# Kernel tuning notes

Measured on AMD Instinct MI355X. Metric: run time of the kernel, lower is better.

Reference implementation:

```python
import jax, jax.numpy as jnp
import numpy as np

B, N, HID = 1, 2048, 1024
H, WK, WV = 16, 64, 64
DH = HID // H  # 64


def setup_inputs() -> dict:
    key = jax.random.key(0)
    ks = jax.random.split(key, 10)
    s = 0.02
    return {
        "hidden_states": jax.random.normal(ks[0], (B, N, HID), jnp.float32),
        "attention_mask": jnp.ones((B, N), jnp.float32),
        "Wq": jax.random.normal(ks[1], (HID, HID), jnp.float32) * s,
        "bq": jnp.zeros((HID,), jnp.float32),
        "Wk": jax.random.normal(ks[2], (HID, HID), jnp.float32) * s,
        "bk": jnp.zeros((HID,), jnp.float32),
        "Wv": jax.random.normal(ks[3], (HID, HID), jnp.float32) * s,
        "bv": jnp.zeros((HID,), jnp.float32),
        # Conv1D(2*WK+1, DH, bias=False): weight [nx=DH, nf=2*WK+1]
        "W_rel_k": jax.random.normal(ks[4], (DH, 2 * WK + 1), jnp.float32) * s,
        # relative_pos_val: [2*WV+1, DH]
        "W_rel_v": jax.random.normal(ks[5], (2 * WV + 1, DH), jnp.float32) * s,
    }


def _attention(hidden_states, attention_mask, Wq, bq, Wk, bk, Wv, bv, W_rel_k, W_rel_v):
    b, n, _ = hidden_states.shape

    def heads(x):  # [B,N,HID] -> [B,H,N,DH]
        return x.reshape(b, n, H, DH).transpose(0, 2, 1, 3)

    q = heads(hidden_states @ Wq + bq)
    k = heads(hidden_states @ Wk + bk)
    v = heads(hidden_states @ Wv + bv)

    scores = jnp.einsum("bhid,bhjd->bhij", q, k)  # [B,H,N,N]

    # --- relative-position key bias: bias[i, j] = q_i . w_{j-i+WK} for |j-i|<=WK ---
    a_k = jnp.einsum("bhid,dw->bhiw", q, W_rel_k)  # [B,H,N,2*WK+1]
    rows = jnp.arange(n)
    slot = rows[None, :] - rows[:, None] + WK       # [N,N] relative slot j-i+WK
    valid_k = (slot >= 0) & (slot <= 2 * WK)
    bias = a_k[:, :, rows[:, None], jnp.clip(slot, 0, 2 * WK)]  # [B,H,N,N]
    scores = scores + jnp.where(valid_k, bias, 0.0)

    scores = scores / np.float32(np.sqrt(DH))  # temperature == 1.0

    # extended attention mask: (1 - mask) * dtype_min added to scores
    ext = (1.0 - attention_mask)[:, None, None, :] * jnp.finfo(scores.dtype).min
    scores = scores + ext

    probs = jax.nn.softmax(scores, axis=-1)  # [B,H,N,N]

    ctx = jnp.einsum("bhij,bhjd->bhid", probs, v)  # [B,H,N,DH]

    # --- relative-position value: band[i, r] = probs[i, i-WV+r]; ctx += band @ W_rel_v ---
    offs = jnp.arange(2 * WV + 1)
    kpos = rows[:, None] - WV + offs[None, :]       # [N, 2*WV+1] absolute key position
    valid_v = (kpos >= 0) & (kpos < n)
    band = probs[:, :, rows[:, None], jnp.clip(kpos, 0, n - 1)]  # [B,H,N,2*WV+1]
    band = jnp.where(valid_v, band, 0.0)
    ctx = ctx + jnp.einsum("bhiw,wd->bhid", band, W_rel_v)

    # merge heads -> [B,N,HID]
    return ctx.transpose(0, 2, 1, 3).reshape(b, n, HID)


def reference(hidden_states, attention_mask, Wq, bq, Wk, bk, Wv, bv, W_rel_k, W_rel_v):
    return _attention(hidden_states, attention_mask, Wq, bq, Wk, bk, Wv, bv, W_rel_k, W_rel_v)
```

## Files before the change

kernel.cpp:

```cpp
#include <hip/hip_runtime.h>
#include <hip/hip_bf16.h>

#define NSEQ 2048
#define HIDDIM 1024
#define NH 16
#define DHEAD 64
#define NW 129
#define AKS 132

typedef float          f32x4 __attribute__((ext_vector_type(4)));
typedef _Float16       f16x4 __attribute__((ext_vector_type(4)));
typedef _Float16       f16x8 __attribute__((ext_vector_type(8)));
typedef unsigned short u16x8 __attribute__((ext_vector_type(8)));
typedef unsigned short u16;

__device__ __forceinline__ float b2f(u16 u){ return __uint_as_float(((unsigned)u) << 16); }
__device__ __forceinline__ float ld_any(const void* p, long idx, int flag){
  return flag ? b2f(((const u16*)p)[idx]) : ((const float*)p)[idx];
}

#define GLOAD_LDS16(gp, lp) \
  __builtin_amdgcn_global_load_lds((const __attribute__((address_space(1))) unsigned int*)(gp), \
                                   (__attribute__((address_space(3))) unsigned int*)(lp), 16, 0, 0)

static const size_t OFF_Q    = 0;
static const size_t OFF_K    = (size_t)4  << 20;
static const size_t OFF_VT   = (size_t)8  << 20;
static const size_t OFF_WT   = (size_t)12 << 20;
static const size_t OFF_AK   = (size_t)18 << 20;
static const size_t OFF_M    = OFF_AK + (size_t)NH * NSEQ * AKS * 4;
static const size_t OFF_L    = OFF_M + (size_t)2 * NH * NSEQ * 4;
static const size_t OFF_CTXP = OFF_L + (size_t)2 * NH * NSEQ * 4;
static const size_t OFF_HSF  = OFF_CTXP + (size_t)2 * NSEQ * HIDDIM * 4;
static const size_t OFF_BIAS = OFF_HSF + (size_t)NSEQ * HIDDIM * 2;
static const size_t OFF_WRK  = OFF_BIAS + 3 * 1024 * 4;
static const size_t OFF_WRV  = OFF_WRK + (size_t)DHEAD * NW * 4;
static const size_t OFF_EXT  = OFF_WRV + (size_t)NW * DHEAD * 4;
static const size_t OFF_FLAG = OFF_EXT + (size_t)NSEQ * 4;

__global__ void detect_kernel(const unsigned* __restrict__ mask_raw, int* __restrict__ flagp){
  *flagp = (mask_raw[0] == 0x3F800000u) ? 0 : 1;
}

__global__ void cvt_hs_kernel(const void* __restrict__ hs, const int* __restrict__ flagp,
                              _Float16* __restrict__ hsf){
  const int flag = *flagp;
  const long base = (long)(blockIdx.x * 256 + threadIdx.x) * 8;
  f16x8 o;
  if (flag){
    const u16* b = (const u16*)hs;
#pragma unroll
    for (int e = 0; e < 8; e++) o[e] = (_Float16)b2f(b[base + e]);
  } else {
    const float* f = (const float*)hs;
#pragma unroll
    for (int e = 0; e < 8; e++) o[e] = (_Float16)f[base + e];
  }
  *(f16x8*)(hsf + base) = o;
}

__global__ void cvt_small_kernel(const void* __restrict__ bq, const void* __restrict__ bk,
                                 const void* __restrict__ bv, const void* __restrict__ wrk,
                                 const void* __restrict__ wrv, const void* __restrict__ mask,
                                 const int* __restrict__ flagp,
                                 float* __restrict__ biasf, float* __restrict__ wrkf,
                                 float* __restrict__ wrvf, float* __restrict__ extf){
  const int flag = *flagp;
  const int idx = blockIdx.x * 256 + threadIdx.x;
  if (idx < 1024)            biasf[idx] = ld_any(bq, idx, flag);
  else if (idx < 2048)       biasf[idx] = ld_any(bk, idx - 1024, flag);
  else if (idx < 3072)       biasf[idx] = ld_any(bv, idx - 2048, flag);
  else if (idx < 3072 + 8256)  wrkf[idx - 3072]  = ld_any(wrk, idx - 3072, flag);
  else if (idx < 3072 + 16512) wrvf[idx - 11328] = ld_any(wrv, idx - 11328, flag);
  else if (idx < 3072 + 16512 + 2048)
    extf[idx - 19584] = (1.f - ld_any(mask, idx - 19584, flag)) * -1.0e30f;
}

__global__ void wtrans_kernel(const void* __restrict__ Wq, const void* __restrict__ Wk,
                              const void* __restrict__ Wv, const int* __restrict__ flagp,
                              _Float16* __restrict__ Wt){
  __shared__ __attribute__((aligned(16))) _Float16 tile[64][65];
  const int flag = *flagp;
  const int z = blockIdx.z;
  const void* src = (z == 0) ? Wq : ((z == 1) ? Wk : Wv);
  _Float16* dst = Wt + (size_t)z * 1024 * 1024;
  const int o0 = blockIdx.x * 64, k0 = blockIdx.y * 64;
  const int t = threadIdx.x;
#pragma unroll
  for (int c = 0; c < 2; c++){
    int idx = t + 256 * c;
    int r = idx >> 3, c8 = (idx & 7) * 8;
    long off = (long)(k0 + r) * 1024 + o0 + c8;
#pragma unroll
    for (int e = 0; e < 8; e++) tile[r][c8 + e] = (_Float16)ld_any(src, off + e, flag);
  }
  __syncthreads();
#pragma unroll
  for (int c = 0; c < 2; c++){
    int idx = t + 256 * c;
    int orow = idx >> 3, k8 = (idx & 7) * 8;
    f16x8 v;
#pragma unroll
    for (int e = 0; e < 8; e++) v[e] = tile[k8 + e][orow];
    *(f16x8*)(dst + (size_t)(o0 + orow) * 1024 + k0 + k8) = v;
  }
}

__launch_bounds__(256, 2)
__global__ void qkv_kernel(const _Float16* __restrict__ hsf, const _Float16* __restrict__ Wt,
                           const float* __restrict__ biasf,
                           _Float16* __restrict__ Qf, _Float16* __restrict__ Kf,
                           _Float16* __restrict__ Vtf){
  __shared__ __attribute__((aligned(16))) _Float16 As[128 * 40];
  __shared__ __attribute__((aligned(16))) _Float16 Bs[128 * 40];
  const int z = blockIdx.z;
  const _Float16* Wz = Wt + (size_t)z * 1024 * 1024;
  const int o0 = blockIdx.x * 128, m0 = blockIdx.y * 128;
  const int t = threadIdx.x, lane = t & 63, wave = t >> 6;
  const int wm = wave >> 1, wn = wave & 1;
  const int q = lane >> 4, ln = lane & 15;
  f32x4 acc[4][4];
#pragma unroll
  for (int a = 0; a < 4; a++)
#pragma unroll
    for (int b = 0; b < 4; b++) acc[a][b] = (f32x4){0.f, 0.f, 0.f, 0.f};

  for (int k0 = 0; k0 < 1024; k0 += 32){
#pragma unroll
    for (int c = 0; c < 2; c++){
      int idx = t + 256 * c;
      int r = idx >> 2, col = (idx & 3) * 8;
      *(f16x8*)&As[r * 40 + col] = *(const f16x8*)(hsf + (size_t)(m0 + r) * 1024 + k0 + col);
      *(f16x8*)&Bs[r * 40 + col] = *(const f16x8*)(Wz + (size_t)(o0 + r) * 1024 + k0 + col);
    }
    __syncthreads();
    f16x8 af[4], bf[4];
#pragma unroll
    for (int mt = 0; mt < 4; mt++) af[mt] = *(const f16x8*)&As[(wm * 64 + mt * 16 + ln) * 40 + q * 8];
#pragma unroll
    for (int nt = 0; nt < 4; nt++) bf[nt] = *(const f16x8*)&Bs[(wn * 64 + nt * 16 + ln) * 40 + q * 8];
#pragma unroll
    for (int mt = 0; mt < 4; mt++)
#pragma unroll
      for (int nt = 0; nt < 4; nt++)
        acc[mt][nt] = __builtin_amdgcn_mfma_f32_16x16x32_f16(af[mt], bf[nt], acc[mt][nt], 0, 0, 0);
    __syncthreads();
  }
#pragma unroll
  for (int nt = 0; nt < 4; nt++){
    int o = o0 + wn * 64 + nt * 16 + ln;
    float bval = biasf[z * 1024 + o];
    int hh = o >> 6, dd = o & 63;
#pragma unroll
    for (int mt = 0; mt < 4; mt++){
      int nb = m0 + wm * 64 + mt * 16 + q * 4;
      if (z == 2){
        f16x4 pk;
#pragma unroll
        for (int r = 0; r < 4; r++) pk[r] = (_Float16)(acc[mt][nt][r] + bval);
        *(f16x4*)(Vtf + (size_t)(hh * 64 + dd) * 2048 + nb) = pk;
      } else {
        _Float16* dstp = (z == 0) ? Qf : Kf;
#pragma unroll
        for (int r = 0; r < 4; r++)
          dstp[(size_t)(hh * 2048 + nb + r) * 64 + dd] = (_Float16)(acc[mt][nt][r] + bval);
      }
    }
  }
}

__launch_bounds__(256, 2)
__global__ void ak_kernel(const _Float16* __restrict__ Qf, const float* __restrict__ wrkf,
                          float* __restrict__ ak){
  __shared__ __attribute__((aligned(16))) _Float16 WrkT[144 * 72];
  const int h = blockIdx.y;
  const int i0 = blockIdx.x * 128;
  const int t = threadIdx.x, lane = t & 63, wave = t >> 6;
  const int q = lane >> 4, ln = lane & 15;
  for (int c = 0; c < 36; c++){
    int idx = t + 256 * c;
    int w = idx >> 6, d = idx & 63;
    float v = (w < NW) ? wrkf[d * NW + w] : 0.f;
    WrkT[w * 72 + d] = (_Float16)v;
  }
  __syncthreads();
  f16x8 afr[2][2];
#pragma unroll
  for (int mt = 0; mt < 2; mt++){
    int row = i0 + wave * 32 + mt * 16 + ln;
#pragma unroll
    for (int ks = 0; ks < 2; ks++)
      afr[mt][ks] = *(const f16x8*)(Qf + (size_t)(h * 2048 + row) * 64 + ks * 32 + q * 8);
  }
  f32x4 acc[2][9];
#pragma unroll
  for (int a = 0; a < 2; a++)
#pragma unroll
    for (int b = 0; b < 9; b++) acc[a][b] = (f32x4){0.f, 0.f, 0.f, 0.f};
#pragma unroll
  for (int nt = 0; nt < 9; nt++){
    f16x8 bfr0 = *(const f16x8*)&WrkT[(nt * 16 + ln) * 72 + q * 8];
    f16x8 bfr1 = *(const f16x8*)&WrkT[(nt * 16 + ln) * 72 + 32 + q * 8];
#pragma unroll
    for (int mt = 0; mt < 2; mt++){
      acc[mt][nt] = __builtin_amdgcn_mfma_f32_16x16x32_f16(afr[mt][0], bfr0, acc[mt][nt], 0, 0, 0);
      acc[mt][nt] = __builtin_amdgcn_mfma_f32_16x16x32_f16(afr[mt][1], bfr1, acc[mt][nt], 0, 0, 0);
    }
  }
#pragma unroll
  for (int nt = 0; nt < 9; nt++){
    int w = nt * 16 + ln;
    if (w > 128) continue;
#pragma unroll
    for (int mt = 0; mt < 2; mt++){
      int ib = i0 + wave * 32 + mt * 16 + q * 4;
#pragma unroll
      for (int r = 0; r < 4; r++)
        ak[(size_t)(h * 2048 + ib + r) * AKS + w] = acc[mt][nt][r];
    }
  }
}

__launch_bounds__(256, 4)
__global__ void flash_kernel(const float* __restrict__ extf,
                             const _Float16* __restrict__ Qf, const _Float16* __restrict__ Kf,
                             const _Float16* __restrict__ Vtf, float* akm,
                             float* __restrict__ ctxpart, float* __restrict__ mws,
                             float* __restrict__ lws){
  __shared__ __attribute__((aligned(16))) _Float16 Ks[2 * 64 * 64];
  __shared__ __attribute__((aligned(16))) _Float16 Vts[2 * 64 * 64];
  __shared__ __attribute__((aligned(16))) float Exts[1024];
  const int h = blockIdx.x, qt = blockIdx.y, jh = blockIdx.z;
  const int t = threadIdx.x, lane = t & 63, wave = t >> 6;
  const int q = lane >> 4, ln = lane & 15;
  const int ibase = qt * 64 + wave * 16;
  const int i = ibase + ln;

  auto stage = [&](int nb, int jn){
#pragma unroll
    for (int s2 = 0; s2 < 2; s2++){
      const int g = s2 * 256 + t;
      const int row = g >> 3, slot = g & 7;
      const int col8 = slot ^ (row & 7);
      const _Float16* gK = Kf + (((size_t)(h * 2048 + jn + row)) << 6) + (col8 << 3);
      const _Float16* gV = Vtf + (((size_t)(h * 64 + row)) << 11) + jn + (col8 << 3);
      _Float16* lK = (_Float16*)Ks + nb * 4096 + ((s2 * 4 + wave) << 9);
      _Float16* lV = (_Float16*)Vts + nb * 4096 + ((s2 * 4 + wave) << 9);
      GLOAD_LDS16(gK, lK);
      GLOAD_LDS16(gV, lV);
    }
  };

  f16x8 qfrag[2];
  {
    const _Float16* qrow = Qf + (size_t)(h * 2048 + i) * 64;
    qfrag[0] = *(const f16x8*)(qrow + q * 8);
    qfrag[1] = *(const f16x8*)(qrow + 32 + q * 8);
  }
  f32x4 accc[4];
#pragma unroll
  for (int dt = 0; dt < 4; dt++) accc[dt] = (f32x4){0.f, 0.f, 0.f, 0.f};
  float m_i = -1.0e30f, l_i = 0.f;
  float* akrow = akm + (size_t)(h * 2048 + i) * AKS;

#pragma unroll
  for (int c2 = 0; c2 < 4; c2++) Exts[t + 256 * c2] = extf[jh * 1024 + t + 256 * c2];
  stage(0, jh * 1024);
  __syncthreads();

  int cur = 0;
  for (int jt = 0; jt < 16; ++jt){
    const int j0 = jh * 1024 + jt * 64;
    if (jt < 15) stage(cur ^ 1, j0 + 64);

    const _Float16* KsC = (const _Float16*)Ks + cur * 4096;
    const _Float16* VsC = (const _Float16*)Vts + cur * 4096;

    f32x4 s[4];
    __builtin_amdgcn_s_setprio(1);
#pragma unroll
    for (int mt = 0; mt < 4; mt++){
      const int row = mt * 16 + ln, rs = row & 7;
      f16x8 kf0 = *(const f16x8*)&KsC[(row << 6) + ((q ^ rs) << 3)];
      f16x8 kf1 = *(const f16x8*)&KsC[(row << 6) + (((q + 4) ^ rs) << 3)];
      f32x4 zz = (f32x4){0.f, 0.f, 0.f, 0.f};
      zz = __builtin_amdgcn_mfma_f32_16x16x32_f16(kf0, qfrag[0], zz, 0, 0, 0);
      zz = __builtin_amdgcn_mfma_f32_16x16x32_f16(kf1, qfrag[1], zz, 0, 0, 0);
      s[mt] = zz;
    }
    __builtin_amdgcn_s_setprio(0);

    const bool band = (j0 <= ibase + 79) && (j0 + 63 >= ibase - 64);
#pragma unroll
    for (int mt = 0; mt < 4; mt++){
      f32x4 ev = *(const f32x4*)&Exts[jt * 64 + mt * 16 + (q << 2)];
#pragma unroll
      for (int r = 0; r < 4; r++){
        float x = s[mt][r];
        int w = j0 + mt * 16 + (q << 2) + r - i + 64;
        if (band && (unsigned)w <= 128u){
          x = (x + akrow[w]) * 0.125f + ev[r];
          akrow[w] = x;
        } else {
          x = x * 0.125f + ev[r];
        }
        s[mt][r] = x;
      }
    }

    float tmax = -1.0e30f;
#pragma unroll
    for (int mt = 0; mt < 4; mt++)
#pragma unroll
      for (int r = 0; r < 4; r++) tmax = fmaxf(tmax, s[mt][r]);
    tmax = fmaxf(tmax, __shfl_xor(tmax, 16, 64));
    tmax = fmaxf(tmax, __shfl_xor(tmax, 32, 64));
    float mnew = fmaxf(m_i, tmax);
    if (!__all(tmax <= m_i)){
      float alpha = __expf(m_i - mnew);
      l_i *= alpha;
#pragma unroll
      for (int dt = 0; dt < 4; dt++)
#pragma unroll
        for (int r = 0; r < 4; r++) accc[dt][r] *= alpha;
    }
    m_i = mnew;
    float tsum = 0.f;
    f16x4 pf[4];
#pragma unroll
    for (int mt = 0; mt < 4; mt++)
#pragma unroll
      for (int r = 0; r < 4; r++){
        float p = __expf(s[mt][r] - mnew);
        tsum += p;
        pf[mt][r] = (_Float16)p;
      }
    tsum += __shfl_xor(tsum, 16, 64);
    tsum += __shfl_xor(tsum, 32, 64);
    l_i += tsum;

    __builtin_amdgcn_s_setprio(1);
#pragma unroll
    for (int dt = 0; dt < 4; dt++){
      const int d = dt * 16 + ln, ds7 = d & 7;
#pragma unroll
      for (int ks = 0; ks < 4; ks++){
        const int c8 = ((ks << 1) | (q >> 1)) ^ ds7;
        f16x4 vf = *(const f16x4*)&VsC[(d << 6) + (c8 << 3) + ((q & 1) << 2)];
        accc[dt] = __builtin_amdgcn_mfma_f32_16x16x16f16(vf, pf[ks], accc[dt], 0, 0, 0);
      }
    }
    __builtin_amdgcn_s_setprio(0);

    __syncthreads();
    cur ^= 1;
  }

  float* cdst = ctxpart + (size_t)jh * NSEQ * HIDDIM;
#pragma unroll
  for (int dt = 0; dt < 4; dt++)
    *(f32x4*)(cdst + (size_t)i * 1024 + h * 64 + dt * 16 + q * 4) = accc[dt];
  if (q == 0){
    mws[jh * NH * NSEQ + h * 2048 + i] = m_i;
    lws[jh * NH * NSEQ + h * 2048 + i] = l_i;
  }
}

__launch_bounds__(256, 2)
__global__ void finish_kernel(const float* __restrict__ sband, const float* __restrict__ mws,
                              const float* __restrict__ lws, const float* __restrict__ wrvf,
                              const float* __restrict__ ctxpart, float* __restrict__ out){
  __shared__ __attribute__((aligned(16))) _Float16 WrvT[64 * 144];
  __shared__ __attribute__((aligned(16))) _Float16 pT[144 * 72];
  __shared__ __attribute__((aligned(16))) float sM[64], sIL[64], sC0[64], sC1[64];
  const int qt = blockIdx.x, h = blockIdx.y;
  const int i0 = qt * 64;
  const int t = threadIdx.x, lane = t & 63, wave = t >> 6;
  const int q = lane >> 4, ln = lane & 15;
  for (int c = 0; c < 36; c++){
    int idx = c * 256 + t;
    int w = idx >> 6, d = idx & 63;
    WrvT[d * 144 + w] = (w < NW) ? (_Float16)wrvf[w * 64 + d] : (_Float16)0.f;
  }
  if (t < 64){
    int i = i0 + t;
    float m0 = mws[h * 2048 + i],            m1 = mws[NH * NSEQ + h * 2048 + i];
    float l0 = lws[h * 2048 + i],            l1 = lws[NH * NSEQ + h * 2048 + i];
    float M = fmaxf(m0, m1);
    float a0 = __expf(m0 - M), a1 = __expf(m1 - M);
    float L = a0 * l0 + a1 * l1;
    float iL = 1.f / L;
    sM[t] = M; sIL[t] = iL; sC0[t] = a0 * iL; sC1[t] = a1 * iL;
  }
  __syncthreads();
  for (int ii = 0; ii < 16; ii++){
    int il = wave * 16 + ii;
    float Mv = sM[il], ILv = sIL[il];
    const float* srow = sband + (size_t)(h * 2048 + i0 + il) * AKS;
#pragma unroll
    for (int c = 0; c < 3; c++){
      int w = lane + 64 * c;
      if (w < 144){
        float p = (w < NW) ? __expf(srow[w] - Mv) * ILv : 0.f;
        pT[w * 72 + il] = (_Float16)p;
      }
    }
  }
  __syncthreads();
  f32x4 acc[4];
#pragma unroll
  for (int mt = 0; mt < 4; mt++) acc[mt] = (f32x4){0.f, 0.f, 0.f, 0.f};
#pragma unroll
  for (int ks = 0; ks < 9; ks++){
    f16x4 bfr;
#pragma unroll
    for (int j = 0; j < 4; j++) bfr[j] = pT[(ks * 16 + q * 4 + j) * 72 + wave * 16 + ln];
#pragma unroll
    for (int mt = 0; mt < 4; mt++){
      f16x4 afr = *(const f16x4*)&WrvT[(mt * 16 + ln) * 144 + ks * 16 + q * 4];
      acc[mt] = __builtin_amdgcn_mfma_f32_16x16x16f16(afr, bfr, acc[mt], 0, 0, 0);
    }
  }
  const int i = i0 + wave * 16 + ln;
  const float c0 = sC0[wave * 16 + ln], c1 = sC1[wave * 16 + ln];
  const float* p0 = ctxpart;
  const float* p1 = ctxpart + (size_t)NSEQ * HIDDIM;
#pragma unroll
  for (int mt = 0; mt < 4; mt++){
    size_t off = (size_t)i * 1024 + h * 64 + mt * 16 + q * 4;
    f32x4 A0 = *(const f32x4*)(p0 + off);
    f32x4 A1 = *(const f32x4*)(p1 + off);
    f32x4 o4;
#pragma unroll
    for (int r = 0; r < 4; r++) o4[r] = c0 * A0[r] + c1 * A1[r] + acc[mt][r];
    *(f32x4*)(out + off) = o4;
  }
}

extern "C" void kernel_launch(void* const* d_in, const int* in_sizes, int n_in,
                              void* d_out, int out_size, void* d_ws, size_t ws_size,
                              hipStream_t stream){
  const void* hs   = d_in[0];
  const void* mask = d_in[1];
  const void* Wq   = d_in[2];
  const void* bq   = d_in[3];
  const void* Wk   = d_in[4];
  const void* bk   = d_in[5];
  const void* Wv   = d_in[6];
  const void* bv   = d_in[7];
  const void* Wrk  = d_in[8];
  const void* Wrv  = d_in[9];
  float* out = (float*)d_out;

  char* ws = (char*)d_ws;
  _Float16* Qf    = (_Float16*)(ws + OFF_Q);
  _Float16* Kf    = (_Float16*)(ws + OFF_K);
  _Float16* Vtf   = (_Float16*)(ws + OFF_VT);
  _Float16* Wt    = (_Float16*)(ws + OFF_WT);
  float*    akp   = (float*)   (ws + OFF_AK);
  float*    mp    = (float*)   (ws + OFF_M);
  float*    lp    = (float*)   (ws + OFF_L);
  float*    ctxp  = (float*)   (ws + OFF_CTXP);
  _Float16* hsf   = (_Float16*)(ws + OFF_HSF);
  float*    biasf = (float*)   (ws + OFF_BIAS);
  float*    wrkf  = (float*)   (ws + OFF_WRK);
  float*    wrvf  = (float*)   (ws + OFF_WRV);
  float*    extf  = (float*)   (ws + OFF_EXT);
  int*      flagp = (int*)     (ws + OFF_FLAG);

  detect_kernel   <<<dim3(1),          1,   0, stream>>>((const unsigned*)mask, flagp);
  cvt_hs_kernel   <<<dim3(1024),       256, 0, stream>>>(hs, flagp, hsf);
  cvt_small_kernel<<<dim3(85),         256, 0, stream>>>(bq, bk, bv, Wrk, Wrv, mask, flagp,
                                                         biasf, wrkf, wrvf, extf);
  wtrans_kernel   <<<dim3(16, 16, 3),  256, 0, stream>>>(Wq, Wk, Wv, flagp, Wt);
  qkv_kernel      <<<dim3(8, 16, 3),   256, 0, stream>>>(hsf, Wt, biasf, Qf, Kf, Vtf);
  ak_kernel       <<<dim3(16, 16),     256, 0, stream>>>(Qf, wrkf, akp);
  flash_kernel    <<<dim3(16, 32, 2),  256, 0, stream>>>(extf, Qf, Kf, Vtf, akp, ctxp, mp, lp);
  finish_kernel   <<<dim3(32, 16),     256, 0, stream>>>(akp, mp, lp, wrvf, ctxp, out);
}
```

Before: 208.0 us.

## Pipeline QKV GEMM with async LDS loads and split flash keys four ways

The QKV GEMM moves to direct global-to-LDS double-buffered loads with 64-row tiles and MFMA priority hints. The 1/sqrt(d) scale is folded into Q at projection time, which removes per-score multiplies in the flash kernel. The flash kernel now uses 512-thread blocks over 128 query rows and splits keys into four chunks, with the finish kernel merging four partials. A fast path skips band logic for off-band tiles, and the workspace is re-laid out so the weight and half-precision input buffers alias the context partial region.

```diff
diff --git a/kernel.cpp b/kernel.cpp
--- a/kernel.cpp
+++ b/kernel.cpp
@@ -7,11 +7,11 @@
 #define DHEAD 64
 #define NW 129
 #define AKS 132
+#define NSPLIT 4
 
 typedef float          f32x4 __attribute__((ext_vector_type(4)));
 typedef _Float16       f16x4 __attribute__((ext_vector_type(4)));
 typedef _Float16       f16x8 __attribute__((ext_vector_type(8)));
-typedef unsigned short u16x8 __attribute__((ext_vector_type(8)));
 typedef unsigned short u16;
 
 __device__ __forceinline__ float b2f(u16 u){ return __uint_as_float(((unsigned)u) << 16); }
@@ -26,13 +26,13 @@
 static const size_t OFF_Q    = 0;
 static const size_t OFF_K    = (size_t)4  << 20;
 static const size_t OFF_VT   = (size_t)8  << 20;
-static const size_t OFF_WT   = (size_t)12 << 20;
-static const size_t OFF_AK   = (size_t)18 << 20;
+static const size_t OFF_AK   = (size_t)12 << 20;
 static const size_t OFF_M    = OFF_AK + (size_t)NH * NSEQ * AKS * 4;
-static const size_t OFF_L    = OFF_M + (size_t)2 * NH * NSEQ * 4;
-static const size_t OFF_CTXP = OFF_L + (size_t)2 * NH * NSEQ * 4;
-static const size_t OFF_HSF  = OFF_CTXP + (size_t)2 * NSEQ * HIDDIM * 4;
-static const size_t OFF_BIAS = OFF_HSF + (size_t)NSEQ * HIDDIM * 2;
+static const size_t OFF_L    = OFF_M + (size_t)NSPLIT * NH * NSEQ * 4;
+static const size_t OFF_CTXP = OFF_L + (size_t)NSPLIT * NH * NSEQ * 4;
+static const size_t OFF_WT   = OFF_CTXP;
+static const size_t OFF_HSF  = OFF_CTXP + ((size_t)6 << 20);
+static const size_t OFF_BIAS = OFF_CTXP + (size_t)NSPLIT * NSEQ * HIDDIM * 4;
 static const size_t OFF_WRK  = OFF_BIAS + 3 * 1024 * 4;
 static const size_t OFF_WRV  = OFF_WRK + (size_t)DHEAD * NW * 4;
 static const size_t OFF_EXT  = OFF_WRV + (size_t)NW * DHEAD * 4;
@@ -106,54 +106,74 @@
   }
 }
 
-__launch_bounds__(256, 2)
+__launch_bounds__(256, 3)
 __global__ void qkv_kernel(const _Float16* __restrict__ hsf, const _Float16* __restrict__ Wt,
                            const float* __restrict__ biasf,
                            _Float16* __restrict__ Qf, _Float16* __restrict__ Kf,
                            _Float16* __restrict__ Vtf){
-  __shared__ __attribute__((aligned(16))) _Float16 As[128 * 40];
-  __shared__ __attribute__((aligned(16))) _Float16 Bs[128 * 40];
+  __shared__ __attribute__((aligned(16))) _Float16 As[2 * 64 * 32];
+  __shared__ __attribute__((aligned(16))) _Float16 Bs[2 * 128 * 32];
   const int z = blockIdx.z;
   const _Float16* Wz = Wt + (size_t)z * 1024 * 1024;
-  const int o0 = blockIdx.x * 128, m0 = blockIdx.y * 128;
+  const int o0 = blockIdx.x * 128, m0 = blockIdx.y * 64;
   const int t = threadIdx.x, lane = t & 63, wave = t >> 6;
   const int wm = wave >> 1, wn = wave & 1;
   const int q = lane >> 4, ln = lane & 15;
-  f32x4 acc[4][4];
-#pragma unroll
-  for (int a = 0; a < 4; a++)
+
+  auto stage = [&](int nb, int k0){
+    {
+      const int row = t >> 2, chunk = t & 3;
+      const _Float16* gA = hsf + (size_t)(m0 + row) * 1024 + k0 + chunk * 8;
+      _Float16* lA = (_Float16*)As + nb * 2048 + (wave << 9);
+      GLOAD_LDS16(gA, lA);
+    }
+#pragma unroll
+    for (int p = 0; p < 2; p++){
+      const int idx = p * 256 + t;
+      const int row = idx >> 2, chunk = idx & 3;
+      const _Float16* gB = Wz + (size_t)(o0 + row) * 1024 + k0 + chunk * 8;
+      _Float16* lB = (_Float16*)Bs + nb * 4096 + ((p * 4 + wave) << 9);
+      GLOAD_LDS16(gB, lB);
+    }
+  };
+
+  f32x4 acc[2][4];
+#pragma unroll
+  for (int a = 0; a < 2; a++)
 #pragma unroll
     for (int b = 0; b < 4; b++) acc[a][b] = (f32x4){0.f, 0.f, 0.f, 0.f};
 
+  stage(0, 0);
+  __syncthreads();
+  int cur = 0;
   for (int k0 = 0; k0 < 1024; k0 += 32){
-#pragma unroll
-    for (int c = 0; c < 2; c++){
-      int idx = t + 256 * c;
-      int r = idx >> 2, col = (idx & 3) * 8;
-      *(f16x8*)&As[r * 40 + col] = *(const f16x8*)(hsf + (size_t)(m0 + r) * 1024 + k0 + col);
-      *(f16x8*)&Bs[r * 40 + col] = *(const f16x8*)(Wz + (size_t)(o0 + r) * 1024 + k0 + col);
-    }
-    __syncthreads();
-    f16x8 af[4], bf[4];
-#pragma unroll
-    for (int mt = 0; mt < 4; mt++) af[mt] = *(const f16x8*)&As[(wm * 64 + mt * 16 + ln) * 40 + q * 8];
-#pragma unroll
-    for (int nt = 0; nt < 4; nt++) bf[nt] = *(const f16x8*)&Bs[(wn * 64 + nt * 16 + ln) * 40 + q * 8];
-#pragma unroll
-    for (int mt = 0; mt < 4; mt++)
+    if (k0 + 32 < 1024) stage(cur ^ 1, k0 + 32);
+    const _Float16* Ac = (const _Float16*)As + cur * 2048;
+    const _Float16* Bc = (const _Float16*)Bs + cur * 4096;
+    f16x8 af[2], bf[4];
+#pragma unroll
+    for (int mt = 0; mt < 2; mt++) af[mt] = *(const f16x8*)&Ac[(wm * 32 + mt * 16 + ln) * 32 + q * 8];
+#pragma unroll
+    for (int nt = 0; nt < 4; nt++) bf[nt] = *(const f16x8*)&Bc[(wn * 64 + nt * 16 + ln) * 32 + q * 8];
+    __builtin_amdgcn_s_setprio(1);
+#pragma unroll
+    for (int mt = 0; mt < 2; mt++)
 #pragma unroll
       for (int nt = 0; nt < 4; nt++)
         acc[mt][nt] = __builtin_amdgcn_mfma_f32_16x16x32_f16(af[mt], bf[nt], acc[mt][nt], 0, 0, 0);
+    __builtin_amdgcn_s_setprio(0);
     __syncthreads();
-  }
+    cur ^= 1;
+  }
+  const float sc = (z == 0) ? 0.125f : 1.0f;
 #pragma unroll
   for (int nt = 0; nt < 4; nt++){
     int o = o0 + wn * 64 + nt * 16 + ln;
     float bval = biasf[z * 1024 + o];
     int hh = o >> 6, dd = o & 63;
 #pragma unroll
-    for (int mt = 0; mt < 4; mt++){
-      int nb = m0 + wm * 64 + mt * 16 + q * 4;
+    for (int mt = 0; mt < 2; mt++){
+      int nb = m0 + wm * 32 + mt * 16 + q * 4;
       if (z == 2){
         f16x4 pk;
 #pragma unroll
@@ -163,7 +183,7 @@
         _Float16* dstp = (z == 0) ? Qf : Kf;
 #pragma unroll
         for (int r = 0; r < 4; r++)
-          dstp[(size_t)(hh * 2048 + nb + r) * 64 + dd] = (_Float16)(acc[mt][nt][r] + bval);
+          dstp[(size_t)(hh * 2048 + nb + r) * 64 + dd] = (_Float16)((acc[mt][nt][r] + bval) * sc);
       }
     }
   }
@@ -221,7 +241,7 @@
   }
 }
 
-__launch_bounds__(256, 4)
+__launch_bounds__(512, 8)
 __global__ void flash_kernel(const float* __restrict__ extf,
                              const _Float16* __restrict__ Qf, const _Float16* __restrict__ Kf,
                              const _Float16* __restrict__ Vtf, float* akm,
@@ -229,26 +249,22 @@
                              float* __restrict__ lws){
   __shared__ __attribute__((aligned(16))) _Float16 Ks[2 * 64 * 64];
   __shared__ __attribute__((aligned(16))) _Float16 Vts[2 * 64 * 64];
-  __shared__ __attribute__((aligned(16))) float Exts[1024];
+  __shared__ __attribute__((aligned(16))) float Exts[512];
   const int h = blockIdx.x, qt = blockIdx.y, jh = blockIdx.z;
   const int t = threadIdx.x, lane = t & 63, wave = t >> 6;
   const int q = lane >> 4, ln = lane & 15;
-  const int ibase = qt * 64 + wave * 16;
+  const int ibase = qt * 128 + wave * 16;
   const int i = ibase + ln;
 
   auto stage = [&](int nb, int jn){
-#pragma unroll
-    for (int s2 = 0; s2 < 2; s2++){
-      const int g = s2 * 256 + t;
-      const int row = g >> 3, slot = g & 7;
-      const int col8 = slot ^ (row & 7);
-      const _Float16* gK = Kf + (((size_t)(h * 2048 + jn + row)) << 6) + (col8 << 3);
-      const _Float16* gV = Vtf + (((size_t)(h * 64 + row)) << 11) + jn + (col8 << 3);
-      _Float16* lK = (_Float16*)Ks + nb * 4096 + ((s2 * 4 + wave) << 9);
-      _Float16* lV = (_Float16*)Vts + nb * 4096 + ((s2 * 4 + wave) << 9);
-      GLOAD_LDS16(gK, lK);
-      GLOAD_LDS16(gV, lV);
-    }
+    const int row = t >> 3, slot = t & 7;
+    const int col8 = slot ^ (row & 7);
+    const _Float16* gK = Kf + (((size_t)(h * 2048 + jn + row)) << 6) + (col8 << 3);
+    const _Float16* gV = Vtf + (((size_t)(h * 64 + row)) << 11) + jn + (col8 << 3);
+    _Float16* lK = (_Float16*)Ks + nb * 4096 + (wave << 9);
+    _Float16* lV = (_Float16*)Vts + nb * 4096 + (wave << 9);
+    GLOAD_LDS16(gK, lK);
+    GLOAD_LDS16(gV, lV);
   };
 
   f16x8 qfrag[2];
@@ -263,15 +279,14 @@
   float m_i = -1.0e30f, l_i = 0.f;
   float* akrow = akm + (size_t)(h * 2048 + i) * AKS;
 
-#pragma unroll
-  for (int c2 = 0; c2 < 4; c2++) Exts[t + 256 * c2] = extf[jh * 1024 + t + 256 * c2];
-  stage(0, jh * 1024);
+  Exts[t] = extf[jh * 512 + t];
+  stage(0, jh * 512);
   __syncthreads();
 
   int cur = 0;
-  for (int jt = 0; jt < 16; ++jt){
-    const int j0 = jh * 1024 + jt * 64;
-    if (jt < 15) stage(cur ^ 1, j0 + 64);
+  for (int jt = 0; jt < 8; ++jt){
+    const int j0 = jh * 512 + jt * 64;
+    if (jt < 7) stage(cur ^ 1, j0 + 64);
 
     const _Float16* KsC = (const _Float16*)Ks + cur * 4096;
     const _Float16* VsC = (const _Float16*)Vts + cur * 4096;
@@ -291,20 +306,29 @@
     __builtin_amdgcn_s_setprio(0);
 
     const bool band = (j0 <= ibase + 79) && (j0 + 63 >= ibase - 64);
-#pragma unroll
-    for (int mt = 0; mt < 4; mt++){
-      f32x4 ev = *(const f32x4*)&Exts[jt * 64 + mt * 16 + (q << 2)];
-#pragma unroll
-      for (int r = 0; r < 4; r++){
-        float x = s[mt][r];
-        int w = j0 + mt * 16 + (q << 2) + r - i + 64;
-        if (band && (unsigned)w <= 128u){
-          x = (x + akrow[w]) * 0.125f + ev[r];
-          akrow[w] = x;
-        } else {
-          x = x * 0.125f + ev[r];
+    if (band){
+#pragma unroll
+      for (int mt = 0; mt < 4; mt++){
+        f32x4 ev = *(const f32x4*)&Exts[jt * 64 + mt * 16 + (q << 2)];
+#pragma unroll
+        for (int r = 0; r < 4; r++){
+          float x = s[mt][r];
+          int w = j0 + mt * 16 + (q << 2) + r - i + 64;
+          if ((unsigned)w <= 128u){
+            x = x + akrow[w] + ev[r];
+            akrow[w] = x;
+          } else {
+            x = x + ev[r];
+          }
+          s[mt][r] = x;
         }
-        s[mt][r] = x;
+      }
+    } else {
+#pragma unroll
+      for (int mt = 0; mt < 4; mt++){
+        f32x4 ev = *(const f32x4*)&Exts[jt * 64 + mt * 16 + (q << 2)];
+#pragma unroll
+        for (int r = 0; r < 4; r++) s[mt][r] += ev[r];
       }
     }
 
@@ -372,7 +396,7 @@
                               const float* __restrict__ ctxpart, float* __restrict__ out){
   __shared__ __attribute__((aligned(16))) _Float16 WrvT[64 * 144];
   __shared__ __attribute__((aligned(16))) _Float16 pT[144 * 72];
-  __shared__ __attribute__((aligned(16))) float sM[64], sIL[64], sC0[64], sC1[64];
+  __shared__ __attribute__((aligned(16))) float sM[64], sIL[64], sC[NSPLIT][64];
   const int qt = blockIdx.x, h = blockIdx.y;
   const int i0 = qt * 64;
   const int t = threadIdx.x, lane = t & 63, wave = t >> 6;
@@ -384,13 +408,20 @@
   }
   if (t < 64){
     int i = i0 + t;
-    float m0 = mws[h * 2048 + i],            m1 = mws[NH * NSEQ + h * 2048 + i];
-    float l0 = lws[h * 2048 + i],            l1 = lws[NH * NSEQ + h * 2048 + i];
-    float M = fmaxf(m0, m1);
-    float a0 = __expf(m0 - M), a1 = __expf(m1 - M);
-    float L = a0 * l0 + a1 * l1;
+    float mv[NSPLIT], lv[NSPLIT];
+#pragma unroll
+    for (int jj = 0; jj < NSPLIT; jj++){
+      mv[jj] = mws[jj * NH * NSEQ + h * 2048 + i];
+      lv[jj] = lws[jj * NH * NSEQ + h * 2048 + i];
+    }
+    float M = fmaxf(fmaxf(mv[0], mv[1]), fmaxf(mv[2], mv[3]));
+    float L = 0.f, a[NSPLIT];
+#pragma unroll
+    for (int jj = 0; jj < NSPLIT; jj++){ a[jj] = __expf(mv[jj] - M); L += a[jj] * lv[jj]; }
     float iL = 1.f / L;
-    sM[t] = M; sIL[t] = iL; sC0[t] = a0 * iL; sC1[t] = a1 * iL;
+    sM[t] = M; sIL[t] = iL;
+#pragma unroll
+    for (int jj = 0; jj < NSPLIT; jj++) sC[jj][t] = a[jj] * iL;
   }
   __syncthreads();
   for (int ii = 0; ii < 16; ii++){
@@ -422,17 +453,18 @@
     }
   }
   const int i = i0 + wave * 16 + ln;
-  const float c0 = sC0[wave * 16 + ln], c1 = sC1[wave * 16 + ln];
-  const float* p0 = ctxpart;
-  const float* p1 = ctxpart + (size_t)NSEQ * HIDDIM;
+  const int il = wave * 16 + ln;
+  const float c0 = sC[0][il], c1 = sC[1][il], c2 = sC[2][il], c3 = sC[3][il];
 #pragma unroll
   for (int mt = 0; mt < 4; mt++){
     size_t off = (size_t)i * 1024 + h * 64 + mt * 16 + q * 4;
-    f32x4 A0 = *(const f32x4*)(p0 + off);
-    f32x4 A1 = *(const f32x4*)(p1 + off);
+    f32x4 A0 = *(const f32x4*)(ctxpart + off);
+    f32x4 A1 = *(const f32x4*)(ctxpart + (size_t)NSEQ * HIDDIM + off);
+    f32x4 A2 = *(const f32x4*)(ctxpart + (size_t)2 * NSEQ * HIDDIM + off);
+    f32x4 A3 = *(const f32x4*)(ctxpart + (size_t)3 * NSEQ * HIDDIM + off);
     f32x4 o4;
 #pragma unroll
-    for (int r = 0; r < 4; r++) o4[r] = c0 * A0[r] + c1 * A1[r] + acc[mt][r];
+    for (int r = 0; r < 4; r++) o4[r] = c0 * A0[r] + c1 * A1[r] + c2 * A2[r] + c3 * A3[r] + acc[mt][r];
     *(f32x4*)(out + off) = o4;
   }
 }
@@ -473,8 +505,8 @@
   cvt_small_kernel<<<dim3(85),         256, 0, stream>>>(bq, bk, bv, Wrk, Wrv, mask, flagp,
                                                          biasf, wrkf, wrvf, extf);
   wtrans_kernel   <<<dim3(16, 16, 3),  256, 0, stream>>>(Wq, Wk, Wv, flagp, Wt);
-  qkv_kernel      <<<dim3(8, 16, 3),   256, 0, stream>>>(hsf, Wt, biasf, Qf, Kf, Vtf);
+  qkv_kernel      <<<dim3(8, 32, 3),   256, 0, stream>>>(hsf, Wt, biasf, Qf, Kf, Vtf);
   ak_kernel       <<<dim3(16, 16),     256, 0, stream>>>(Qf, wrkf, akp);
-  flash_kernel    <<<dim3(16, 32, 2),  256, 0, stream>>>(extf, Qf, Kf, Vtf, akp, ctxp, mp, lp);
+  flash_kernel    <<<dim3(16, 16, 4),  512, 0, stream>>>(extf, Qf, Kf, Vtf, akp, ctxp, mp, lp);
   finish_kernel   <<<dim3(32, 16),     256, 0, stream>>>(akp, mp, lp, wrvf, ctxp, out);
 }
```

After: 260.0 us. 25.0% more time.
